# Performance work log

Measured on AMD Instinct MI355X. Metric: run time of the kernel, lower is better.

Reference implementation:

```python
import jax, jax.numpy as jnp
import numpy as np
from jax import lax

B, T, V, D, H, C = 256, 1024, 5000, 100, 64, 2


def setup_inputs() -> dict:
    key = jax.random.key(0)
    k0, k1, k2, k3, k4 = jax.random.split(key, 5)
    tokens = jax.random.randint(k0, (B, T), 0, V)  # 0 is the mask/pad id
    E = jax.random.normal(k1, (V, D), dtype=jnp.float32) * 0.05
    W = jax.random.normal(k2, (D, H), dtype=jnp.float32) * (1.0 / np.sqrt(D))
    U = jax.random.normal(k3, (H, H), dtype=jnp.float32) * (1.0 / np.sqrt(H))
    b = jnp.zeros((H,), dtype=jnp.float32)
    Wd = jax.random.normal(k4, (H, C), dtype=jnp.float32) * (1.0 / np.sqrt(H))
    bd = jnp.zeros((C,), dtype=jnp.float32)
    return {"tokens": tokens, "E": E, "W": W, "U": U, "b": b, "Wd": Wd, "bd": bd}


def reference(tokens, E, W, U, b, Wd, bd):
    # Embedding with mask_zero=True: mask where token != 0
    x = E[tokens]                      # [B, T, D]
    mask = tokens != 0                 # [B, T] bool
    # Precompute input projection for all timesteps (batched GEMM).
    xW = jnp.einsum('btd,dh->bth', x, W) + b  # [B, T, H]

    def step(h, inp):
        xw_t, m_t = inp                # xw_t: [B,H], m_t: [B]
        h_new = jnp.tanh(xw_t + h @ U)
        # Keras masked recurrence: masked steps carry previous state/output.
        h = jnp.where(m_t[:, None], h_new, h)
        return h, h

    h0 = jnp.zeros((tokens.shape[0], U.shape[0]), dtype=xW.dtype)
    _, hs = lax.scan(step, h0, (jnp.swapaxes(xW, 0, 1), mask.T))  # hs: [T, B, H]
    hs = jnp.swapaxes(hs, 0, 1)        # [B, T, H]
    pooled = jnp.mean(hs, axis=1)      # tf.reduce_mean over time (unmasked mean)
    # Dropout is identity at inference.
    logits = pooled @ Wd + bd
    return jax.nn.sigmoid(logits)
```

## Files before the change

### kernel.cpp

```cpp
#include <hip/hip_runtime.h>

#define B_ 256
#define T_ 1024
#define V_ 5000
#define D_ 100
#define H_ 64
#define C_ 2

__global__ __launch_bounds__(256) void ew_kernel(const float* __restrict__ E,
                                                 const float* __restrict__ W,
                                                 const float* __restrict__ bias,
                                                 float* __restrict__ EW) {
    int idx = blockIdx.x * 256 + threadIdx.x;
    if (idx >= V_ * H_) return;
    int h = idx & (H_ - 1);
    int v = idx >> 6;
    float acc = bias[h];
    const float* Erow = E + v * D_;
    #pragma unroll 4
    for (int d = 0; d < D_; ++d) {
        acc = fmaf(Erow[d], W[d * H_ + h], acc);
    }
    EW[idx] = acc;
}

__device__ __forceinline__ float readlane_f(float v, int lane) {
    return __uint_as_float(__builtin_amdgcn_readlane(__float_as_uint(v), lane));
}

__global__ __launch_bounds__(64, 1) void rnn_kernel(const int* __restrict__ tokens,
                                                    const float* __restrict__ EW,
                                                    const float* __restrict__ U,
                                                    const float* __restrict__ Wd,
                                                    const float* __restrict__ bd,
                                                    float* __restrict__ out) {
    const int b = blockIdx.x;
    const int j = threadIdx.x;

    __shared__ float4 sh_U4[H_ * 16];
    __shared__ int    sh_tok[T_ + 2];

    float* sh_Uf = (float*)sh_U4;
    #pragma unroll 8
    for (int i = 0; i < H_; ++i) {
        float u = U[i * H_ + j];
        int p = ((i >> 2) + j) & 15;
        sh_Uf[(j << 6) + (p << 2) + (i & 3)] = u;
    }
    const int* tok = tokens + b * T_;
    #pragma unroll
    for (int k = 0; k < T_ / H_; ++k) {
        sh_tok[k * H_ + j] = tok[k * H_ + j];
    }
    if (j < 2) sh_tok[T_ + j] = 0;
    __syncthreads();

    int uidx[16];
    #pragma unroll
    for (int c = 0; c < 16; ++c) uidx[c] = (j << 4) + ((c + j) & 15);

    float h = 0.f;
    float pooled = 0.f;

    int2 tkA = *(const int2*)&sh_tok[0];
    float xw0 = EW[tkA.x * H_ + j];
    float xw1 = EW[tkA.y * H_ + j];

    #define RNN_STEP(tokv, xwv)                                          \
    {                                                                    \
        float a0 = 0.f, a1 = 0.f, a2 = 0.f, a3 = 0.f;                    \
        _Pragma("unroll")                                                \
        for (int c = 0; c < 16; ++c) {                                   \
            const float4 u4 = sh_U4[uidx[c]];                            \
            a0 = fmaf(readlane_f(h, 4 * c + 0), u4.x, a0);               \
            a1 = fmaf(readlane_f(h, 4 * c + 1), u4.y, a1);               \
            a2 = fmaf(readlane_f(h, 4 * c + 2), u4.z, a2);               \
            a3 = fmaf(readlane_f(h, 4 * c + 3), u4.w, a3);               \
        }                                                                \
        float x = ((a0 + a1) + (a2 + a3)) + (xwv);                       \
        float e = __expf(2.f * x);                                       \
        float r = __builtin_amdgcn_rcpf(e + 1.f);                        \
        float hn = fmaf(-2.f, r, 1.f);                                   \
        h = ((tokv) != 0) ? hn : h;                                      \
        pooled += h;                                                     \
    }

    for (int t = 0; t < T_; t += 2) {
        int2 tkB = *(const int2*)&sh_tok[t + 2];
        float xw2 = EW[tkB.x * H_ + j];
        float xw3 = EW[tkB.y * H_ + j];

        RNN_STEP(tkA.x, xw0);
        RNN_STEP(tkA.y, xw1);

        tkA = tkB;
        xw0 = xw2;
        xw1 = xw3;
    }
    #undef RNN_STEP

    float p = pooled * (1.0f / (float)T_);
    float v0 = p * Wd[j * C_ + 0];
    float v1 = p * Wd[j * C_ + 1];
    #pragma unroll
    for (int off = 32; off >= 1; off >>= 1) {
        v0 += __shfl_down(v0, off, 64);
        v1 += __shfl_down(v1, off, 64);
    }
    if (j == 0) {
        float l0 = v0 + bd[0];
        float l1 = v1 + bd[1];
        out[b * C_ + 0] = 1.f / (1.f + __expf(-l0));
        out[b * C_ + 1] = 1.f / (1.f + __expf(-l1));
    }
}

extern "C" void kernel_launch(void* const* d_in, const int* in_sizes, int n_in,
                              void* d_out, int out_size, void* d_ws, size_t ws_size,
                              hipStream_t stream) {
    const int*   tokens = (const int*)  d_in[0];
    const float* E      = (const float*)d_in[1];
    const float* W      = (const float*)d_in[2];
    const float* U      = (const float*)d_in[3];
    const float* bias   = (const float*)d_in[4];
    const float* Wd     = (const float*)d_in[5];
    const float* bd     = (const float*)d_in[6];
    float* out = (float*)d_out;
    float* EW  = (float*)d_ws;

    ew_kernel<<<(V_ * H_ + 255) / 256, 256, 0, stream>>>(E, W, bias, EW);
    rnn_kernel<<<B_, H_, 0, stream>>>(tokens, EW, U, Wd, bd, out);
}
```

Before: 309.9 us.

## Split recurrent matvec across four waves with per-step LDS reduction

The RNN kernel now launches 256 threads per batch row instead of 64. Each of the four waves computes the partial h·U dot product over 16 of the 64 inputs, so each wave does 16 readlanes instead of 64. The partials are written to a double-buffered LDS array, synchronised with a block barrier, and summed redundantly by every wave before the tanh. This shortens the serial per-step chain but adds a barrier and an LDS write/read round trip on every timestep.

```diff
diff --git a/kernel.cpp b/kernel.cpp
--- a/kernel.cpp
+++ b/kernel.cpp
@@ -28,36 +28,45 @@
     return __uint_as_float(__builtin_amdgcn_readlane(__float_as_uint(v), lane));
 }
 
-__global__ __launch_bounds__(64, 1) void rnn_kernel(const int* __restrict__ tokens,
-                                                    const float* __restrict__ EW,
-                                                    const float* __restrict__ U,
-                                                    const float* __restrict__ Wd,
-                                                    const float* __restrict__ bd,
-                                                    float* __restrict__ out) {
-    const int b = blockIdx.x;
-    const int j = threadIdx.x;
+__global__ __launch_bounds__(256, 1) void rnn_kernel(const int* __restrict__ tokens,
+                                                     const float* __restrict__ EW,
+                                                     const float* __restrict__ U,
+                                                     const float* __restrict__ Wd,
+                                                     const float* __restrict__ bd,
+                                                     float* __restrict__ out) {
+    const int b   = blockIdx.x;
+    const int tid = threadIdx.x;
+    const int w   = tid >> 6;
+    const int j   = tid & 63;
 
-    __shared__ float4 sh_U4[H_ * 16];
+    __shared__ float4 sh_U4[4 * H_ * 4];
+    __shared__ float  sh_p[2 * 4 * H_];
     __shared__ int    sh_tok[T_ + 2];
 
     float* sh_Uf = (float*)sh_U4;
-    #pragma unroll 8
-    for (int i = 0; i < H_; ++i) {
-        float u = U[i * H_ + j];
-        int p = ((i >> 2) + j) & 15;
-        sh_Uf[(j << 6) + (p << 2) + (i & 3)] = u;
+    #pragma unroll
+    for (int c = 0; c < 4; ++c) {
+        int slot = (c + (j >> 1)) & 3;
+        #pragma unroll
+        for (int r = 0; r < 4; ++r) {
+            int i = (w << 4) + (c << 2) + r;
+            sh_Uf[((((w << 6) + j) << 4)) + (slot << 2) + r] = U[i * H_ + j];
+        }
     }
     const int* tok = tokens + b * T_;
     #pragma unroll
-    for (int k = 0; k < T_ / H_; ++k) {
-        sh_tok[k * H_ + j] = tok[k * H_ + j];
+    for (int k = 0; k < T_ / 256; ++k) {
+        sh_tok[k * 256 + tid] = tok[k * 256 + tid];
     }
-    if (j < 2) sh_tok[T_ + j] = 0;
+    if (tid < 2) sh_tok[T_ + tid] = 0;
     __syncthreads();
 
-    int uidx[16];
+    int uaddr[4];
     #pragma unroll
-    for (int c = 0; c < 16; ++c) uidx[c] = (j << 4) + ((c + j) & 15);
+    for (int c = 0; c < 4; ++c)
+        uaddr[c] = (((w << 6) + j) << 2) + ((c + (j >> 1)) & 3);
+    const int ibase = w << 4;
+    const int pw    = (w << 6) + j;
 
     float h = 0.f;
     float pooled = 0.f;
@@ -66,18 +75,25 @@
     float xw0 = EW[tkA.x * H_ + j];
     float xw1 = EW[tkA.y * H_ + j];
 
-    #define RNN_STEP(tokv, xwv)                                          \
+    #define RNN_STEP(buf, tokv, xwv)                                     \
     {                                                                    \
         float a0 = 0.f, a1 = 0.f, a2 = 0.f, a3 = 0.f;                    \
         _Pragma("unroll")                                                \
-        for (int c = 0; c < 16; ++c) {                                   \
-            const float4 u4 = sh_U4[uidx[c]];                            \
-            a0 = fmaf(readlane_f(h, 4 * c + 0), u4.x, a0);               \
-            a1 = fmaf(readlane_f(h, 4 * c + 1), u4.y, a1);               \
-            a2 = fmaf(readlane_f(h, 4 * c + 2), u4.z, a2);               \
-            a3 = fmaf(readlane_f(h, 4 * c + 3), u4.w, a3);               \
+        for (int c = 0; c < 4; ++c) {                                    \
+            const float4 u4 = sh_U4[uaddr[c]];                           \
+            int bi = ibase + (c << 2);                                   \
+            a0 = fmaf(readlane_f(h, bi + 0), u4.x, a0);                  \
+            a1 = fmaf(readlane_f(h, bi + 1), u4.y, a1);                  \
+            a2 = fmaf(readlane_f(h, bi + 2), u4.z, a2);                  \
+            a3 = fmaf(readlane_f(h, bi + 3), u4.w, a3);                  \
         }                                                                \
-        float x = ((a0 + a1) + (a2 + a3)) + (xwv);                       \
+        sh_p[(buf) * 256 + pw] = (a0 + a1) + (a2 + a3);                  \
+        __syncthreads();                                                 \
+        float p0 = sh_p[(buf) * 256 + j];                                \
+        float p1 = sh_p[(buf) * 256 + 64 + j];                           \
+        float p2 = sh_p[(buf) * 256 + 128 + j];                          \
+        float p3 = sh_p[(buf) * 256 + 192 + j];                          \
+        float x = ((p0 + p1) + (p2 + p3)) + (xwv);                       \
         float e = __expf(2.f * x);                                       \
         float r = __builtin_amdgcn_rcpf(e + 1.f);                        \
         float hn = fmaf(-2.f, r, 1.f);                                   \
@@ -90,8 +106,8 @@
         float xw2 = EW[tkB.x * H_ + j];
         float xw3 = EW[tkB.y * H_ + j];
 
-        RNN_STEP(tkA.x, xw0);
-        RNN_STEP(tkA.y, xw1);
+        RNN_STEP(0, tkA.x, xw0);
+        RNN_STEP(1, tkA.y, xw1);
 
         tkA = tkB;
         xw0 = xw2;
@@ -99,19 +115,21 @@
     }
     #undef RNN_STEP
 
-    float p = pooled * (1.0f / (float)T_);
-    float v0 = p * Wd[j * C_ + 0];
-    float v1 = p * Wd[j * C_ + 1];
-    #pragma unroll
-    for (int off = 32; off >= 1; off >>= 1) {
-        v0 += __shfl_down(v0, off, 64);
-        v1 += __shfl_down(v1, off, 64);
-    }
-    if (j == 0) {
-        float l0 = v0 + bd[0];
-        float l1 = v1 + bd[1];
-        out[b * C_ + 0] = 1.f / (1.f + __expf(-l0));
-        out[b * C_ + 1] = 1.f / (1.f + __expf(-l1));
+    if (w == 0) {
+        float p = pooled * (1.0f / (float)T_);
+        float v0 = p * Wd[j * C_ + 0];
+        float v1 = p * Wd[j * C_ + 1];
+        #pragma unroll
+        for (int off = 32; off >= 1; off >>= 1) {
+            v0 += __shfl_down(v0, off, 64);
+            v1 += __shfl_down(v1, off, 64);
+        }
+        if (j == 0) {
+            float l0 = v0 + bd[0];
+            float l1 = v1 + bd[1];
+            out[b * C_ + 0] = 1.f / (1.f + __expf(-l0));
+            out[b * C_ + 1] = 1.f / (1.f + __expf(-l1));
+        }
     }
 }
 
@@ -129,5 +147,5 @@
     float* EW  = (float*)d_ws;
 
     ew_kernel<<<(V_ * H_ + 255) / 256, 256, 0, stream>>>(E, W, bias, EW);
-    rnn_kernel<<<B_, H_, 0, stream>>>(tokens, EW, U, Wd, bd, out);
+    rnn_kernel<<<B_, 256, 0, stream>>>(tokens, EW, U, Wd, bd, out);
 }
```

New measurement: 364.9 us. 17.7% more time.
